# Kernel optimization log

Hardware: AMD Instinct MI355X
Metric: run time of the kernel (lower is better)

The kernel has to match this reference:

```python
import jax, jax.numpy as jnp
import numpy as np

D_OUT, D_IN, RANK = 4096, 4096, 512
BATCH, SEQ = 4, 2048


def setup_inputs() -> dict:
    key = jax.random.key(0)
    kx, ka, kb, kc = jax.random.split(key, 4)
    x = jax.random.normal(kx, (BATCH, SEQ, D_IN), dtype=jnp.float32)
    # CP/low-rank factors: weight = A @ B.T, shape [D_OUT, D_IN]
    A = jax.random.normal(ka, (D_OUT, RANK), dtype=jnp.float32) * (1.0 / np.sqrt(RANK))
    B = jax.random.normal(kb, (D_IN, RANK), dtype=jnp.float32) * (1.0 / np.sqrt(D_IN))
    bias = jax.random.normal(kc, (D_OUT,), dtype=jnp.float32)
    return {"x": x, "A": A, "B": B, "bias": bias}


def reference(x, A, B, bias):
    # method == 'cp_2d': reconstruct weight then apply F.linear
    weight = A @ B.T                      # [D_OUT, D_IN]
    # F.linear(x, W, b) = x @ W.T + b
    out = jnp.einsum('bsd,od->bso', x, weight) + bias
    return out
```

## Files before the change

kernel.cpp:

```cpp
#include <hip/hip_runtime.h>

typedef __attribute__((ext_vector_type(8))) __bf16 bf16x8;
typedef __attribute__((ext_vector_type(4))) __bf16 bf16x4;
typedef __attribute__((ext_vector_type(4))) float f32x4;

#define D_OUT 4096
#define D_IN  4096
#define RANK  512
#define MROWS 8192

__device__ __forceinline__ void gload_lds16(const void* gsrc, void* ldst) {
  __builtin_amdgcn_global_load_lds(
      (const __attribute__((address_space(1))) void*)gsrc,
      (__attribute__((address_space(3))) void*)ldst, 16, 0, 0);
}

__global__ __launch_bounds__(256) void cvt_f32_bf16(const float* __restrict__ in,
                                                    __bf16* __restrict__ out,
                                                    size_t n) {
  size_t i = ((size_t)blockIdx.x * 256 + threadIdx.x) * 4;
  size_t stride = (size_t)gridDim.x * 256 * 4;
  for (; i < n; i += stride) {
    float4 v = *(const float4*)(in + i);
    bf16x4 o = {(__bf16)v.x, (__bf16)v.y, (__bf16)v.z, (__bf16)v.w};
    *(bf16x4*)(out + i) = o;
  }
}

__global__ __launch_bounds__(256) void transpose_cvt(const float* __restrict__ in,
                                                     __bf16* __restrict__ out,
                                                     int R, int C) {
  __shared__ __bf16 tile[64][72];
  const int r0 = blockIdx.x * 64, c0 = blockIdx.y * 64;
  const int t = threadIdx.x;
  const int tr = t / 16, tc4 = (t % 16) * 4;
#pragma unroll
  for (int i = 0; i < 4; ++i) {
    int r = i * 16 + tr;
    float4 v = *(const float4*)(in + (size_t)(r0 + r) * C + c0 + tc4);
    tile[r][tc4 + 0] = (__bf16)v.x;
    tile[r][tc4 + 1] = (__bf16)v.y;
    tile[r][tc4 + 2] = (__bf16)v.z;
    tile[r][tc4 + 3] = (__bf16)v.w;
  }
  __syncthreads();
#pragma unroll
  for (int i = 0; i < 4; ++i) {
    int c = i * 16 + tr;
    bf16x4 o = {tile[tc4 + 0][c], tile[tc4 + 1][c], tile[tc4 + 2][c], tile[tc4 + 3][c]};
    *(bf16x4*)(out + (size_t)(c0 + c) * R + r0 + tc4) = o;
  }
}

template <int BM, int BN, int BK, bool OUT_F32, bool BIAS>
__global__ __launch_bounds__(256) void gemm_bt(const __bf16* __restrict__ Amat,
                                               const __bf16* __restrict__ Bmat,
                                               const float* __restrict__ bias,
                                               void* __restrict__ Cout,
                                               int M, int N, int K) {
  constexpr int WM = BM / 2, WN = BN / 2;
  constexpr int MI = WM / 16, NI = WN / 16;
  __shared__ alignas(16) __bf16 Al[BM * BK];
  __shared__ alignas(16) __bf16 Bl[BN * BK];

  const int tid = threadIdx.x;
  const int wid = tid >> 6;
  const int lane = tid & 63;
  const int l15 = lane & 15, lhi = lane >> 4;
  const int wr = wid >> 1, wc = wid & 1;
  const int m0 = blockIdx.x * BM, n0 = blockIdx.y * BN;

  f32x4 acc[MI][NI] = {};

  for (int k0 = 0; k0 < K; k0 += BK) {
    constexpr int IA = BM * BK / (256 * 8);
#pragma unroll
    for (int it = 0; it < IA; ++it) {
      int o = (it * 256 + tid) * 8;
      int row = o / BK;
      int blk = (o % BK) / 8;
      int col = (blk ^ (row & 7)) * 8;
      gload_lds16(Amat + (size_t)(m0 + row) * K + k0 + col,
                  Al + (it * 256 + wid * 64) * 8);
    }
    constexpr int IB = BN * BK / (256 * 8);
#pragma unroll
    for (int it = 0; it < IB; ++it) {
      int o = (it * 256 + tid) * 8;
      int row = o / BK;
      int blk = (o % BK) / 8;
      int col = (blk ^ (row & 7)) * 8;
      gload_lds16(Bmat + (size_t)(n0 + row) * K + k0 + col,
                  Bl + (it * 256 + wid * 64) * 8);
    }
    __syncthreads();

#pragma unroll
    for (int kk = 0; kk < BK / 32; ++kk) {
      bf16x8 af[MI], bf[NI];
#pragma unroll
      for (int mi = 0; mi < MI; ++mi) {
        int row = wr * WM + mi * 16 + l15;
        int blk = (kk * 4 + lhi) ^ (row & 7);
        af[mi] = *(const bf16x8*)((const char*)Al + row * (BK * 2) + blk * 16);
      }
#pragma unroll
      for (int ni = 0; ni < NI; ++ni) {
        int row = wc * WN + ni * 16 + l15;
        int blk = (kk * 4 + lhi) ^ (row & 7);
        bf[ni] = *(const bf16x8*)((const char*)Bl + row * (BK * 2) + blk * 16);
      }
#pragma unroll
      for (int mi = 0; mi < MI; ++mi)
#pragma unroll
        for (int ni = 0; ni < NI; ++ni)
          acc[mi][ni] = __builtin_amdgcn_mfma_f32_16x16x32_bf16(af[mi], bf[ni],
                                                                acc[mi][ni], 0, 0, 0);
    }
    __syncthreads();
  }

#pragma unroll
  for (int ni = 0; ni < NI; ++ni) {
    int col = n0 + wc * WN + ni * 16 + l15;
    float bv = 0.f;
    if constexpr (BIAS) bv = bias[col];
#pragma unroll
    for (int mi = 0; mi < MI; ++mi) {
#pragma unroll
      for (int r = 0; r < 4; ++r) {
        int row = m0 + wr * WM + mi * 16 + lhi * 4 + r;
        if constexpr (OUT_F32)
          ((float*)Cout)[(size_t)row * N + col] = acc[mi][ni][r] + bv;
        else
          ((__bf16*)Cout)[(size_t)row * N + col] = (__bf16)acc[mi][ni][r];
      }
    }
  }
}

extern "C" void kernel_launch(void* const* d_in, const int* in_sizes, int n_in,
                              void* d_out, int out_size, void* d_ws, size_t ws_size,
                              hipStream_t stream) {
  const float* x    = (const float*)d_in[0];
  const float* A    = (const float*)d_in[1];
  const float* B    = (const float*)d_in[2];
  const float* bias = (const float*)d_in[3];
  float* out = (float*)d_out;

  __bf16* xb = (__bf16*)d_out;
  char* ws = (char*)d_ws;
  __bf16* Ab = (__bf16*)ws;
  __bf16* Bt = (__bf16*)(ws + ((size_t)4 << 20));
  __bf16* Tt = (__bf16*)(ws + ((size_t)8 << 20));

  hipLaunchKernelGGL(cvt_f32_bf16, dim3(2048), dim3(256), 0, stream,
                     x, xb, (size_t)MROWS * D_IN);
  hipLaunchKernelGGL(cvt_f32_bf16, dim3(512), dim3(256), 0, stream,
                     A, Ab, (size_t)D_OUT * RANK);
  hipLaunchKernelGGL(transpose_cvt, dim3(D_IN / 64, RANK / 64), dim3(256), 0, stream,
                     B, Bt, D_IN, RANK);
  hipLaunchKernelGGL((gemm_bt<128, 64, 64, false, false>),
                     dim3(MROWS / 128, RANK / 64), dim3(256), 0, stream,
                     xb, Bt, nullptr, Tt, MROWS, RANK, D_IN);
  hipLaunchKernelGGL((gemm_bt<128, 128, 64, true, true>),
                     dim3(MROWS / 128, D_OUT / 128), dim3(256), 0, stream,
                     Tt, Ab, bias, out, MROWS, D_OUT, RANK);
}
```

Measured before the change: 155.8 us.

## Fuse x fp32-to-bf16 conversion into first GEMM and swizzle block order

```diff
diff --git a/kernel.cpp b/kernel.cpp
--- a/kernel.cpp
+++ b/kernel.cpp
@@ -52,12 +52,11 @@
   }
 }
 
-template <int BM, int BN, int BK, bool OUT_F32, bool BIAS>
-__global__ __launch_bounds__(256) void gemm_bt(const __bf16* __restrict__ Amat,
-                                               const __bf16* __restrict__ Bmat,
-                                               const float* __restrict__ bias,
-                                               void* __restrict__ Cout,
-                                               int M, int N, int K) {
+template <int BM, int BN, int BK>
+__global__ __launch_bounds__(256) void gemm_xf32_bt(const float* __restrict__ Xf,
+                                                    const __bf16* __restrict__ Bmat,
+                                                    __bf16* __restrict__ Cout,
+                                                    int M, int N, int K) {
   constexpr int WM = BM / 2, WN = BN / 2;
   constexpr int MI = WM / 16, NI = WN / 16;
   __shared__ alignas(16) __bf16 Al[BM * BK];
@@ -68,7 +67,112 @@
   const int lane = tid & 63;
   const int l15 = lane & 15, lhi = lane >> 4;
   const int wr = wid >> 1, wc = wid & 1;
-  const int m0 = blockIdx.x * BM, n0 = blockIdx.y * BN;
+
+  const int nwg = gridDim.x * gridDim.y;
+  const int bid = blockIdx.y * gridDim.x + blockIdx.x;
+  const int swz = (bid & 7) * (nwg >> 3) + (bid >> 3);
+  const int m0 = (swz % gridDim.x) * BM;
+  const int n0 = (swz / gridDim.x) * BN;
+
+  f32x4 acc[MI][NI] = {};
+
+  constexpr int IA = BM * BK / (256 * 8);
+  constexpr int IB = BN * BK / (256 * 8);
+
+  for (int k0 = 0; k0 < K; k0 += BK) {
+    float4 av[IA][2];
+#pragma unroll
+    for (int it = 0; it < IA; ++it) {
+      int o = (it * 256 + tid) * 8;
+      int row = o / BK, col = o % BK;
+      const float* src = Xf + (size_t)(m0 + row) * K + k0 + col;
+      av[it][0] = *(const float4*)src;
+      av[it][1] = *(const float4*)(src + 4);
+    }
+#pragma unroll
+    for (int it = 0; it < IB; ++it) {
+      int o = (it * 256 + tid) * 8;
+      int row = o / BK;
+      int blk = (o % BK) / 8;
+      int col = (blk ^ (row & 7)) * 8;
+      gload_lds16(Bmat + (size_t)(n0 + row) * K + k0 + col,
+                  Bl + (it * 256 + wid * 64) * 8);
+    }
+#pragma unroll
+    for (int it = 0; it < IA; ++it) {
+      int o = (it * 256 + tid) * 8;
+      int row = o / BK;
+      int blk = (o % BK) / 8;
+      int swblk = blk ^ (row & 7);
+      bf16x8 w = {(__bf16)av[it][0].x, (__bf16)av[it][0].y,
+                  (__bf16)av[it][0].z, (__bf16)av[it][0].w,
+                  (__bf16)av[it][1].x, (__bf16)av[it][1].y,
+                  (__bf16)av[it][1].z, (__bf16)av[it][1].w};
+      *(bf16x8*)((char*)Al + row * (BK * 2) + swblk * 16) = w;
+    }
+    __syncthreads();
+
+#pragma unroll
+    for (int kk = 0; kk < BK / 32; ++kk) {
+      bf16x8 af[MI], bf[NI];
+#pragma unroll
+      for (int mi = 0; mi < MI; ++mi) {
+        int row = wr * WM + mi * 16 + l15;
+        int blk = (kk * 4 + lhi) ^ (row & 7);
+        af[mi] = *(const bf16x8*)((const char*)Al + row * (BK * 2) + blk * 16);
+      }
+#pragma unroll
+      for (int ni = 0; ni < NI; ++ni) {
+        int row = wc * WN + ni * 16 + l15;
+        int blk = (kk * 4 + lhi) ^ (row & 7);
+        bf[ni] = *(const bf16x8*)((const char*)Bl + row * (BK * 2) + blk * 16);
+      }
+#pragma unroll
+      for (int mi = 0; mi < MI; ++mi)
+#pragma unroll
+        for (int ni = 0; ni < NI; ++ni)
+          acc[mi][ni] = __builtin_amdgcn_mfma_f32_16x16x32_bf16(af[mi], bf[ni],
+                                                                acc[mi][ni], 0, 0, 0);
+    }
+    __syncthreads();
+  }
+
+#pragma unroll
+  for (int ni = 0; ni < NI; ++ni) {
+    int col = n0 + wc * WN + ni * 16 + l15;
+#pragma unroll
+    for (int mi = 0; mi < MI; ++mi) {
+#pragma unroll
+      for (int r = 0; r < 4; ++r) {
+        int row = m0 + wr * WM + mi * 16 + lhi * 4 + r;
+        Cout[(size_t)row * N + col] = (__bf16)acc[mi][ni][r];
+      }
+    }
+  }
+}
+
+template <int BM, int BN, int BK>
+__global__ __launch_bounds__(256) void gemm_bt_bias(const __bf16* __restrict__ Amat,
+                                                    const __bf16* __restrict__ Bmat,
+                                                    const float* __restrict__ bias,
+                                                    float* __restrict__ Cout,
+                                                    int M, int N, int K) {
+  constexpr int WM = BM / 2, WN = BN / 2;
+  constexpr int MI = WM / 16, NI = WN / 16;
+  __shared__ alignas(16) __bf16 Al[BM * BK];
+  __shared__ alignas(16) __bf16 Bl[BN * BK];
+
+  const int tid = threadIdx.x;
+  const int wid = tid >> 6;
+  const int lane = tid & 63;
+  const int l15 = lane & 15, lhi = lane >> 4;
+  const int wr = wid >> 1, wc = wid & 1;
+
+  const int nwg = gridDim.x * gridDim.y;
+  const int bid = blockIdx.y * gridDim.x + blockIdx.x;
+  const int swz = (bid & 7) * (nwg >> 3) + (bid >> 3);
+  const int m0 = (swz % gridDim.x) * BM;
+  const int n0 = (swz / gridDim.x) * BN;
 
   f32x4 acc[MI][NI] = {};
 
@@ -123,17 +227,13 @@
 #pragma unroll
   for (int ni = 0; ni < NI; ++ni) {
     int col = n0 + wc * WN + ni * 16 + l15;
-    float bv = 0.f;
-    if constexpr (BIAS) bv = bias[col];
+    float bv = bias[col];
 #pragma unroll
     for (int mi = 0; mi < MI; ++mi) {
 #pragma unroll
       for (int r = 0; r < 4; ++r) {
         int row = m0 + wr * WM + mi * 16 + lhi * 4 + r;
-        if constexpr (OUT_F32)
-          ((float*)Cout)[(size_t)row * N + col] = acc[mi][ni][r] + bv;
-        else
-          ((__bf16*)Cout)[(size_t)row * N + col] = (__bf16)acc[mi][ni][r];
+        Cout[(size_t)row * N + col] = acc[mi][ni][r] + bv;
       }
     }
   }
@@ -148,22 +248,19 @@
   const float* bias = (const float*)d_in[3];
   float* out = (float*)d_out;
 
-  __bf16* xb = (__bf16*)d_out;
   char* ws = (char*)d_ws;
   __bf16* Ab = (__bf16*)ws;
   __bf16* Bt = (__bf16*)(ws + ((size_t)4 << 20));
   __bf16* Tt = (__bf16*)(ws + ((size_t)8 << 20));
 
-  hipLaunchKernelGGL(cvt_f32_bf16, dim3(2048), dim3(256), 0, stream,
-                     x, xb, (size_t)MROWS * D_IN);
   hipLaunchKernelGGL(cvt_f32_bf16, dim3(512), dim3(256), 0, stream,
                      A, Ab, (size_t)D_OUT * RANK);
   hipLaunchKernelGGL(transpose_cvt, dim3(D_IN / 64, RANK / 64), dim3(256), 0, stream,
                      B, Bt, D_IN, RANK);
-  hipLaunchKernelGGL((gemm_bt<128, 64, 64, false, false>),
+  hipLaunchKernelGGL((gemm_xf32_bt<128, 64, 64>),
                      dim3(MROWS / 128, RANK / 64), dim3(256), 0, stream,
-                     xb, Bt, nullptr, Tt, MROWS, RANK, D_IN);
-  hipLaunchKernelGGL((gemm_bt<128, 128, 64, true, true>),
+                     x, Bt, Tt, MROWS, RANK, D_IN);
+  hipLaunchKernelGGL((gemm_bt_bias<128, 128, 64>),
                      dim3(MROWS / 128, D_OUT / 128), dim3(256), 0, stream,
                      Tt, Ab, bias, out, MROWS, D_OUT, RANK);
 }
```

Result: slower. 248.3 us (+59.4%).

## Replace second GEMM with 256x256 double-buffered 8-wave phased pipeline kernel

Applied to the files above, without the earlier changes.

```diff
diff --git a/kernel.cpp b/kernel.cpp
--- a/kernel.cpp
+++ b/kernel.cpp
@@ -52,11 +52,10 @@
   }
 }
 
-template <int BM, int BN, int BK, bool OUT_F32, bool BIAS>
+template <int BM, int BN, int BK>
 __global__ __launch_bounds__(256) void gemm_bt(const __bf16* __restrict__ Amat,
                                                const __bf16* __restrict__ Bmat,
-                                               const float* __restrict__ bias,
-                                               void* __restrict__ Cout,
+                                               __bf16* __restrict__ Cout,
                                                int M, int N, int K) {
   constexpr int WM = BM / 2, WN = BN / 2;
   constexpr int MI = WM / 16, NI = WN / 16;
@@ -68,7 +67,13 @@
   const int lane = tid & 63;
   const int l15 = lane & 15, lhi = lane >> 4;
   const int wr = wid >> 1, wc = wid & 1;
-  const int m0 = blockIdx.x * BM, n0 = blockIdx.y * BN;
+
+  const int gx = gridDim.x;
+  const int nwg = gx * gridDim.y;
+  const int bid = blockIdx.y * gx + blockIdx.x;
+  const int swz = (bid & 7) * (nwg >> 3) + (bid >> 3);
+  const int m0 = (swz % gx) * BM;
+  const int n0 = (swz / gx) * BN;
 
   f32x4 acc[MI][NI] = {};
 
@@ -97,7 +102,7 @@
 
 #pragma unroll
     for (int kk = 0; kk < BK / 32; ++kk) {
-      bf16x8 af[MI], bf[NI];
+      bf16x8 af[MI], bfv[NI];
 #pragma unroll
       for (int mi = 0; mi < MI; ++mi) {
         int row = wr * WM + mi * 16 + l15;
@@ -108,13 +113,13 @@
       for (int ni = 0; ni < NI; ++ni) {
         int row = wc * WN + ni * 16 + l15;
         int blk = (kk * 4 + lhi) ^ (row & 7);
-        bf[ni] = *(const bf16x8*)((const char*)Bl + row * (BK * 2) + blk * 16);
+        bfv[ni] = *(const bf16x8*)((const char*)Bl + row * (BK * 2) + blk * 16);
       }
 #pragma unroll
       for (int mi = 0; mi < MI; ++mi)
 #pragma unroll
         for (int ni = 0; ni < NI; ++ni)
-          acc[mi][ni] = __builtin_amdgcn_mfma_f32_16x16x32_bf16(af[mi], bf[ni],
+          acc[mi][ni] = __builtin_amdgcn_mfma_f32_16x16x32_bf16(af[mi], bfv[ni],
                                                                 acc[mi][ni], 0, 0, 0);
     }
     __syncthreads();
@@ -123,17 +128,160 @@
 #pragma unroll
   for (int ni = 0; ni < NI; ++ni) {
     int col = n0 + wc * WN + ni * 16 + l15;
-    float bv = 0.f;
-    if constexpr (BIAS) bv = bias[col];
 #pragma unroll
     for (int mi = 0; mi < MI; ++mi) {
 #pragma unroll
       for (int r = 0; r < 4; ++r) {
         int row = m0 + wr * WM + mi * 16 + lhi * 4 + r;
-        if constexpr (OUT_F32)
-          ((float*)Cout)[(size_t)row * N + col] = acc[mi][ni][r] + bv;
-        else
-          ((__bf16*)Cout)[(size_t)row * N + col] = (__bf16)acc[mi][ni][r];
+        Cout[(size_t)row * N + col] = (__bf16)acc[mi][ni][r];
+      }
+    }
+  }
+}
+
+template <int NT>
+__global__ __launch_bounds__(512, 1) void gemm2_8ph(const __bf16* __restrict__ Amat,
+                                                    const __bf16* __restrict__ Bmat,
+                                                    const float* __restrict__ bias,
+                                                    float* __restrict__ Cout,
+                                                    int M, int N, int K) {
+  __shared__ alignas(16) __bf16 sm[2 * 32768];
+
+  const int tid = threadIdx.x;
+  const int wid = tid >> 6;
+  const int lane = tid & 63;
+  const int l15 = lane & 15, lhi = lane >> 4;
+  const int wr = wid >> 2, wc = wid & 3;
+
+  const int gx = gridDim.x;
+  const int nwg = gx * gridDim.y;
+  const int bid = blockIdx.y * gx + blockIdx.x;
+  const int swz = (bid & 7) * (nwg >> 3) + (bid >> 3);
+  const int m0 = (swz % gx) * 256;
+  const int n0 = (swz / gx) * 256;
+
+  f32x4 acc[8][4] = {};
+  bf16x8 af[4][2];
+  bf16x8 bfr[2][2][2];
+
+#define STAGE(tt, jj) do {                                                        \
+    const __bf16* _src = ((jj) < 2)                                               \
+        ? Amat + (size_t)(m0 + (jj) * 128) * K + (tt) * 64                        \
+        : Bmat + (size_t)(n0 + ((jj)-2) * 128) * K + (tt) * 64;                   \
+    __bf16* _dst = sm + ((tt) & 1) * 32768 +                                      \
+                   (((jj) < 2) ? (jj) * 8192 : 16384 + ((jj)-2) * 8192);          \
+    _Pragma("unroll")                                                             \
+    for (int _it = 0; _it < 2; ++_it) {                                           \
+      int _o = (_it * 512 + tid) * 8;                                             \
+      int _row = _o >> 6;                                                         \
+      int _blk = (_o & 63) >> 3;                                                  \
+      int _col = (_blk ^ (_row & 7)) * 8;                                         \
+      gload_lds16(_src + (size_t)_row * K + _col,                                 \
+                  _dst + (_it * 512 + wid * 64) * 8);                             \
+    }                                                                             \
+  } while (0)
+
+#define LDA8(tt, mh) do {                                                         \
+    const char* _b = (const char*)(sm + ((tt) & 1) * 32768);                      \
+    _Pragma("unroll")                                                             \
+    for (int _mi = 0; _mi < 4; ++_mi)                                             \
+      _Pragma("unroll")                                                           \
+      for (int _kk = 0; _kk < 2; ++_kk) {                                         \
+        int _r = wr * 128 + (mh) * 64 + _mi * 16 + l15;                           \
+        int _blk = (_kk * 4 + lhi) ^ (_r & 7);                                    \
+        af[_mi][_kk] = *(const bf16x8*)(_b + _r * 128 + _blk * 16);               \
+      }                                                                           \
+  } while (0)
+
+#define LDB4(tt, nh) do {                                                         \
+    const char* _b = (const char*)(sm + ((tt) & 1) * 32768 + 16384);              \
+    _Pragma("unroll")                                                             \
+    for (int _ni = 0; _ni < 2; ++_ni)                                             \
+      _Pragma("unroll")                                                           \
+      for (int _kk = 0; _kk < 2; ++_kk) {                                         \
+        int _r = wc * 64 + (nh) * 32 + _ni * 16 + l15;                            \
+        int _blk = (_kk * 4 + lhi) ^ (_r & 7);                                    \
+        bfr[nh][_ni][_kk] = *(const bf16x8*)(_b + _r * 128 + _blk * 16);          \
+      }                                                                           \
+  } while (0)
+
+#define MMA16(mh, nh) do {                                                        \
+    _Pragma("unroll")                                                             \
+    for (int _mi = 0; _mi < 4; ++_mi)                                             \
+      _Pragma("unroll")                                                           \
+      for (int _ni = 0; _ni < 2; ++_ni)                                           \
+        _Pragma("unroll")                                                         \
+        for (int _kk = 0; _kk < 2; ++_kk)                                         \
+          acc[(mh) * 4 + _mi][(nh) * 2 + _ni] =                                   \
+              __builtin_amdgcn_mfma_f32_16x16x32_bf16(                            \
+                  af[_mi][_kk], bfr[nh][_ni][_kk],                                \
+                  acc[(mh) * 4 + _mi][(nh) * 2 + _ni], 0, 0, 0);                  \
+  } while (0)
+
+  STAGE(0, 0); STAGE(0, 1); STAGE(0, 2); STAGE(0, 3);
+  STAGE(1, 0);
+  asm volatile("s_waitcnt vmcnt(2)" ::: "memory");
+  __builtin_amdgcn_s_barrier();
+
+  for (int t = 0; t < NT; ++t) {
+    LDA8(t, 0); LDB4(t, 0);
+    if (t + 1 < NT) STAGE(t + 1, 1);
+    __builtin_amdgcn_s_barrier();
+    asm volatile("s_waitcnt lgkmcnt(0)" ::: "memory");
+    __builtin_amdgcn_sched_barrier(0);
+    __builtin_amdgcn_s_setprio(1);
+    MMA16(0, 0);
+    __builtin_amdgcn_s_setprio(0);
+    __builtin_amdgcn_s_barrier();
+
+    LDB4(t, 1);
+    if (t + 1 < NT) STAGE(t + 1, 2);
+    __builtin_amdgcn_s_barrier();
+    asm volatile("s_waitcnt lgkmcnt(0)" ::: "memory");
+    __builtin_amdgcn_sched_barrier(0);
+    __builtin_amdgcn_s_setprio(1);
+    MMA16(0, 1);
+    __builtin_amdgcn_s_setprio(0);
+    __builtin_amdgcn_s_barrier();
+
+    LDA8(t, 1);
+    if (t + 1 < NT) STAGE(t + 1, 3);
+    __builtin_amdgcn_s_barrier();
+    asm volatile("s_waitcnt lgkmcnt(0)" ::: "memory");
+    __builtin_amdgcn_sched_barrier(0);
+    __builtin_amdgcn_s_setprio(1);
+    MMA16(1, 1);
+    __builtin_amdgcn_s_setprio(0);
+    __builtin_amdgcn_s_barrier();
+
+    if (t + 2 < NT) STAGE(t + 2, 0);
+    __builtin_amdgcn_s_barrier();
+    __builtin_amdgcn_s_setprio(1);
+    MMA16(1, 0);
+    __builtin_amdgcn_s_setprio(0);
+    if (t < NT - 2) {
+      asm volatile("s_waitcnt vmcnt(2)" ::: "memory");
+    } else if (t == NT - 2) {
+      asm volatile("s_waitcnt vmcnt(0)" ::: "memory");
+    }
+    __builtin_amdgcn_s_barrier();
+  }
+
+#undef STAGE
+#undef LDA8
+#undef LDB4
+#undef MMA16
+
+#pragma unroll
+  for (int ni = 0; ni < 4; ++ni) {
+    int col = n0 + wc * 64 + ni * 16 + l15;
+    float bv = bias[col];
+#pragma unroll
+    for (int mi = 0; mi < 8; ++mi) {
+#pragma unroll
+      for (int r = 0; r < 4; ++r) {
+        int row = m0 + wr * 128 + mi * 16 + lhi * 4 + r;
+        Cout[(size_t)row * N + col] = acc[mi][ni][r] + bv;
       }
     }
   }
@@ -160,10 +308,10 @@
                      A, Ab, (size_t)D_OUT * RANK);
   hipLaunchKernelGGL(transpose_cvt, dim3(D_IN / 64, RANK / 64), dim3(256), 0, stream,
                      B, Bt, D_IN, RANK);
-  hipLaunchKernelGGL((gemm_bt<128, 64, 64, false, false>),
+  hipLaunchKernelGGL((gemm_bt<128, 64, 64>),
                      dim3(MROWS / 128, RANK / 64), dim3(256), 0, stream,
-                     xb, Bt, nullptr, Tt, MROWS, RANK, D_IN);
-  hipLaunchKernelGGL((gemm_bt<128, 128, 64, true, true>),
-                     dim3(MROWS / 128, D_OUT / 128), dim3(256), 0, stream,
+                     xb, Bt, Tt, MROWS, RANK, D_IN);
+  hipLaunchKernelGGL((gemm2_8ph<8>),
+                     dim3(MROWS / 256, D_OUT / 256), dim3(512), 0, stream,
                      Tt, Ab, bias, out, MROWS, D_OUT, RANK);
 }
```

Result: slower. 173.7 us (+11.5%).

## Split-K the first low-rank GEMM with larger tiles and add a grid swizzle

Applied to the files above, without the earlier changes.

```diff
diff --git a/kernel.cpp b/kernel.cpp
--- a/kernel.cpp
+++ b/kernel.cpp
@@ -52,12 +52,24 @@
   }
 }
 
+__global__ __launch_bounds__(256) void reduce2_bf16(const __bf16* __restrict__ t0,
+                                                    const __bf16* __restrict__ t1,
+                                                    __bf16* __restrict__ o) {
+  size_t i = ((size_t)blockIdx.x * 256 + threadIdx.x) * 8;
+  bf16x8 a = *(const bf16x8*)(t0 + i);
+  bf16x8 b = *(const bf16x8*)(t1 + i);
+  bf16x8 r;
+#pragma unroll
+  for (int j = 0; j < 8; ++j) r[j] = (__bf16)((float)a[j] + (float)b[j]);
+  *(bf16x8*)(o + i) = r;
+}
+
 template <int BM, int BN, int BK, bool OUT_F32, bool BIAS>
 __global__ __launch_bounds__(256) void gemm_bt(const __bf16* __restrict__ Amat,
                                                const __bf16* __restrict__ Bmat,
                                                const float* __restrict__ bias,
                                                void* __restrict__ Cout,
-                                               int M, int N, int K) {
+                                               int M, int N, int Kred, int ldk) {
   constexpr int WM = BM / 2, WN = BN / 2;
   constexpr int MI = WM / 16, NI = WN / 16;
   __shared__ alignas(16) __bf16 Al[BM * BK];
@@ -68,11 +80,18 @@
   const int lane = tid & 63;
   const int l15 = lane & 15, lhi = lane >> 4;
   const int wr = wid >> 1, wc = wid & 1;
-  const int m0 = blockIdx.x * BM, n0 = blockIdx.y * BN;
+
+  const int gx = gridDim.x;
+  const int nwg = gx * gridDim.y;
+  const int bid = blockIdx.y * gx + blockIdx.x;
+  const int swz = (bid & 7) * (nwg >> 3) + (bid >> 3);
+  const int m0 = (swz % gx) * BM;
+  const int n0 = (swz / gx) * BN;
+  const int kbase = blockIdx.z * Kred;
 
   f32x4 acc[MI][NI] = {};
 
-  for (int k0 = 0; k0 < K; k0 += BK) {
+  for (int k0 = kbase; k0 < kbase + Kred; k0 += BK) {
     constexpr int IA = BM * BK / (256 * 8);
 #pragma unroll
     for (int it = 0; it < IA; ++it) {
@@ -80,7 +99,7 @@
       int row = o / BK;
       int blk = (o % BK) / 8;
       int col = (blk ^ (row & 7)) * 8;
-      gload_lds16(Amat + (size_t)(m0 + row) * K + k0 + col,
+      gload_lds16(Amat + (size_t)(m0 + row) * ldk + k0 + col,
                   Al + (it * 256 + wid * 64) * 8);
     }
     constexpr int IB = BN * BK / (256 * 8);
@@ -90,14 +109,14 @@
       int row = o / BK;
       int blk = (o % BK) / 8;
       int col = (blk ^ (row & 7)) * 8;
-      gload_lds16(Bmat + (size_t)(n0 + row) * K + k0 + col,
+      gload_lds16(Bmat + (size_t)(n0 + row) * ldk + k0 + col,
                   Bl + (it * 256 + wid * 64) * 8);
     }
     __syncthreads();
 
 #pragma unroll
     for (int kk = 0; kk < BK / 32; ++kk) {
-      bf16x8 af[MI], bf[NI];
+      bf16x8 af[MI], bfv[NI];
 #pragma unroll
       for (int mi = 0; mi < MI; ++mi) {
         int row = wr * WM + mi * 16 + l15;
@@ -108,18 +127,19 @@
       for (int ni = 0; ni < NI; ++ni) {
         int row = wc * WN + ni * 16 + l15;
         int blk = (kk * 4 + lhi) ^ (row & 7);
-        bf[ni] = *(const bf16x8*)((const char*)Bl + row * (BK * 2) + blk * 16);
+        bfv[ni] = *(const bf16x8*)((const char*)Bl + row * (BK * 2) + blk * 16);
       }
 #pragma unroll
       for (int mi = 0; mi < MI; ++mi)
 #pragma unroll
         for (int ni = 0; ni < NI; ++ni)
-          acc[mi][ni] = __builtin_amdgcn_mfma_f32_16x16x32_bf16(af[mi], bf[ni],
+          acc[mi][ni] = __builtin_amdgcn_mfma_f32_16x16x32_bf16(af[mi], bfv[ni],
                                                                 acc[mi][ni], 0, 0, 0);
     }
     __syncthreads();
   }
 
+  char* cbase = (char*)Cout + (size_t)blockIdx.z * M * N * (OUT_F32 ? 4 : 2);
 #pragma unroll
   for (int ni = 0; ni < NI; ++ni) {
     int col = n0 + wc * WN + ni * 16 + l15;
@@ -131,9 +151,9 @@
       for (int r = 0; r < 4; ++r) {
         int row = m0 + wr * WM + mi * 16 + lhi * 4 + r;
         if constexpr (OUT_F32)
-          ((float*)Cout)[(size_t)row * N + col] = acc[mi][ni][r] + bv;
+          ((float*)cbase)[(size_t)row * N + col] = acc[mi][ni][r] + bv;
         else
-          ((__bf16*)Cout)[(size_t)row * N + col] = (__bf16)acc[mi][ni][r];
+          ((__bf16*)cbase)[(size_t)row * N + col] = (__bf16)acc[mi][ni][r];
       }
     }
   }
@@ -149,6 +169,7 @@
   float* out = (float*)d_out;
 
   __bf16* xb = (__bf16*)d_out;
+  __bf16* tp = (__bf16*)((char*)d_out + ((size_t)64 << 20));
   char* ws = (char*)d_ws;
   __bf16* Ab = (__bf16*)ws;
   __bf16* Bt = (__bf16*)(ws + ((size_t)4 << 20));
@@ -160,10 +181,12 @@
                      A, Ab, (size_t)D_OUT * RANK);
   hipLaunchKernelGGL(transpose_cvt, dim3(D_IN / 64, RANK / 64), dim3(256), 0, stream,
                      B, Bt, D_IN, RANK);
-  hipLaunchKernelGGL((gemm_bt<128, 64, 64, false, false>),
-                     dim3(MROWS / 128, RANK / 64), dim3(256), 0, stream,
-                     xb, Bt, nullptr, Tt, MROWS, RANK, D_IN);
+  hipLaunchKernelGGL((gemm_bt<128, 128, 64, false, false>),
+                     dim3(MROWS / 128, RANK / 128, 2), dim3(256), 0, stream,
+                     xb, Bt, nullptr, tp, MROWS, RANK, D_IN / 2, D_IN);
+  hipLaunchKernelGGL(reduce2_bf16, dim3(MROWS * RANK / (256 * 8)), dim3(256), 0, stream,
+                     tp, tp + (size_t)MROWS * RANK, Tt);
   hipLaunchKernelGGL((gemm_bt<128, 128, 64, true, true>),
-                     dim3(MROWS / 128, D_OUT / 128), dim3(256), 0, stream,
-                     Tt, Ab, bias, out, MROWS, D_OUT, RANK);
+                     dim3(MROWS / 128, D_OUT / 128, 1), dim3(256), 0, stream,
+                     Tt, Ab, bias, out, MROWS, D_OUT, RANK, RANK);
 }
```

Result: slower. 167.0 us (+7.2%).
